# Kernel optimization log

Measured on AMD Instinct MI355X. Metric: run time of the kernel, lower is better.

The kernel has to match this reference:

```python
import jax, jax.numpy as jnp
import numpy as np

# ---- configuration (from init_kwargs / image geometry) ----
NUM_CLASSES = 10          # digit classes 1..10 (scores has K+1 cols, col 0 = background)
R = 500000                # total digit proposals for the image
T = 2048                  # topk_per_image: fixed-size survivor set for jit-friendly NMS
SCORE_T = 0.05            # digit_score_thresh
NMS_T = 0.5               # nms_thresh
IMG_W, IMG_H = 1920.0, 1080.0
CLS_OFFSET = IMG_W + IMG_H + 1.0  # batched_nms coordinate-offset trick (per-class NMS)


def setup_inputs() -> dict:
    key = jax.random.key(0)
    k1, k2, k3, k4 = jax.random.split(key, 4)
    # realistic boxes: uniform centers over the image, sizes in [10, 100] px
    cxcy = jax.random.uniform(k1, (R, 2)) * jnp.array([IMG_W, IMG_H], dtype=jnp.float32)
    wh = 10.0 + 90.0 * jax.random.uniform(k2, (R, 2))
    boxes = jnp.concatenate([cxcy - 0.5 * wh, cxcy + 0.5 * wh], axis=1)  # [R,4] x1y1x2y2
    # class probabilities over K+1 classes (col 0 = background)
    scores = jax.nn.softmax(jax.random.normal(k3, (R, NUM_CLASSES + 1)), axis=1)
    # per-box digit-center score (pred_digit_center_scores)
    center_scores = jax.random.uniform(k4, (R,))
    return {"boxes": boxes, "scores": scores, "center_scores": center_scores}


def _iou_matrix(b):
    # b: [T,4] in x1y1x2y2. Returns [T,T] pairwise IoU.
    area = jnp.clip(b[:, 2] - b[:, 0], 0.0) * jnp.clip(b[:, 3] - b[:, 1], 0.0)  # [T]
    lt = jnp.maximum(b[:, None, :2], b[None, :, :2])  # [T,T,2]
    rb = jnp.minimum(b[:, None, 2:], b[None, :, 2:])  # [T,T,2]
    wh = jnp.clip(rb - lt, 0.0)
    inter = wh[..., 0] * wh[..., 1]
    return inter / (area[:, None] + area[None, :] - inter + 1e-9)


def reference(boxes, scores, center_scores):
    # 1) drop background column, fuse with digit-center scores
    fg = scores[:, 1:] * center_scores[:, None]            # [R,K]
    # 2) clip boxes to image (Boxes.clip)
    clipped = jnp.stack([
        jnp.clip(boxes[:, 0], 0.0, IMG_W),
        jnp.clip(boxes[:, 1], 0.0, IMG_H),
        jnp.clip(boxes[:, 2], 0.0, IMG_W),
        jnp.clip(boxes[:, 3], 0.0, IMG_H),
    ], axis=1)                                             # [R,4]
    # 3) flatten (box, class) candidates and threshold (filter_mask = scores > thresh)
    flat = fg.reshape(-1)                                  # [R*K]
    masked = jnp.where(flat > SCORE_T, flat, -1.0)
    # 4) fixed-size pre-filter: top-T candidates by fused score
    vals, idx = jax.lax.top_k(masked, T)                   # sorted descending
    cand_boxes = clipped[idx // NUM_CLASSES]               # [T,4]
    cand_cls = idx % NUM_CLASSES                           # [T] (cls_id - 1)
    valid = vals > SCORE_T
    # 5) per-class batched NMS via coordinate-offset trick
    nms_boxes = cand_boxes + cand_cls.astype(cand_boxes.dtype)[:, None] * CLS_OFFSET
    iou = _iou_matrix(nms_boxes)                           # [T,T]
    rng = jnp.arange(T)
    def body(i, keep):
        sup = keep[i] & (iou[i] > NMS_T) & (rng > i)
        return keep & jnp.logical_not(sup)
    keep = jax.lax.fori_loop(0, T, body, valid)            # greedy NMS (inputs sorted by score)
    # 6) masked fixed-shape outputs: kept boxes + kept scores
    out_boxes = jnp.where(keep[:, None], cand_boxes, 0.0)
    out_scores = jnp.where(keep, vals, 0.0)
    return jnp.concatenate([out_boxes, out_scores[:, None]], axis=1)  # [T,5]
```

## Files before the change

### kernel.cpp

```cpp
#include <hip/hip_runtime.h>
#include <stdint.h>

typedef unsigned int u32;
typedef unsigned long long u64;

#define SCORE_THR 0.05f
#define NMS_THR   0.5f
#define TK        2048
#define CAP       4096
#define BASE14    ((int)(0x3D4CCCCDu >> 14))
#define MAGIC11   3123612579ull
#define NREP      8
#define PAIR_CAP  16384
#define SGRID     1024

#define WS_OFFS   0
#define WS_BINPOS 16384
#define WS_HDR    32768
#define WS_CBX    33024
#define WS_NBX    65792
#define WS_VALS   98560
#define WS_HREP   106752
#define WS_BUF    237824
#define WS_PAIRS  269824

__global__ void k_hist(const float* __restrict__ scores,
                       const float* __restrict__ center,
                       int R, u32* __restrict__ hrep) {
    __shared__ u32 h[4096];
    for (int t = threadIdx.x; t < 4096; t += blockDim.x) h[t] = 0;
    __syncthreads();
    int total_e = R * 11;
    int nq = total_e >> 2;
    int qpb = (nq + (int)gridDim.x - 1) / (int)gridDim.x;
    int start = (int)blockIdx.x * qpb;
    int end = start + qpb; if (end > nq) end = nq;
    int bd = (int)blockDim.x;
    for (int q = start + (int)threadIdx.x; q < end; q += 4 * bd) {
        int q1 = q + bd, q2 = q + 2 * bd, q3 = q + 3 * bd;
        float4 va, vb, vc, vd;
        bool ga = true, gb = q1 < end, gc = q2 < end, gd = q3 < end;
        va = ((const float4*)scores)[q];
        if (gb) vb = ((const float4*)scores)[q1];
        if (gc) vc = ((const float4*)scores)[q2];
        if (gd) vd = ((const float4*)scores)[q3];
#define HPROC(g, qq, v4)                                                   \
        if (g) {                                                           \
            float vv[4] = {v4.x, v4.y, v4.z, v4.w};                        \
            _Pragma("unroll")                                              \
            for (int j = 0; j < 4; j++) {                                  \
                u32 e2 = ((u32)(qq) << 2) + (u32)j;                        \
                u32 r = (u32)(((u64)e2 * MAGIC11) >> 35);                  \
                u32 c = e2 - r * 11u;                                      \
                if (c != 0u) {                                             \
                    float s = __fmul_rn(vv[j], center[r]);                 \
                    if (s > SCORE_THR) {                                   \
                        u32 key = __float_as_uint(s);                      \
                        int b = (int)(key >> 14) - BASE14;                 \
                        b = min(max(b, 0), 4095);                          \
                        atomicAdd(&h[b], 1u);                              \
                    }                                                      \
                }                                                          \
            }                                                              \
        }
        HPROC(ga, q, va) HPROC(gb, q1, vb) HPROC(gc, q2, vc) HPROC(gd, q3, vd)
#undef HPROC
    }
    if (blockIdx.x == 0 && threadIdx.x == 0) {
        for (int e2 = nq << 2; e2 < total_e; e2++) {
            u32 r = (u32)(((u64)(u32)e2 * MAGIC11) >> 35);
            u32 c = (u32)e2 - r * 11u;
            if (c != 0u) {
                float s = __fmul_rn(scores[e2], center[r]);
                if (s > SCORE_THR) {
                    u32 key = __float_as_uint(s);
                    int b = (int)(key >> 14) - BASE14;
                    b = min(max(b, 0), 4095);
                    atomicAdd(&h[b], 1u);
                }
            }
        }
    }
    __syncthreads();
    u32* hout = hrep + (size_t)(blockIdx.x & (NREP - 1)) * 4096;
    for (int t = threadIdx.x; t < 4096; t += blockDim.x)
        if (h[t]) atomicAdd(&hout[t], h[t]);
}

__global__ void k_scan(const u32* __restrict__ hrep, u32* __restrict__ offs,
                       u32* hdr) {
    int lane = threadIdx.x;
    int base = 4096 - 64 * (lane + 1);
    u32 v[64];
    u32 segsum = 0;
#pragma unroll
    for (int j = 0; j < 64; j++) {
        u32 s = 0;
#pragma unroll
        for (int i = 0; i < NREP; i++) s += hrep[i * 4096 + base + j];
        v[j] = s; segsum += s;
    }
    u32 incl = segsum;
    for (int off = 1; off < 64; off <<= 1) {
        u32 t = (u32)__shfl_up((int)incl, off);
        if (lane >= off) incl += t;
    }
    u32 excl = incl - segsum;
    u32 total = (u32)__shfl((int)incl, 63);
    u32 run = excl;
#pragma unroll
    for (int j = 63; j >= 0; j--) { offs[base + j] = run; run += v[j]; }
    if (lane == 0) hdr[6] = total;
    if (total < (u32)TK) {
        if (lane == 0) { hdr[3] = 0; hdr[5] = total; }
        return;
    }
    if ((excl < (u32)TK) && (incl >= (u32)TK)) {
        u32 cum = excl;
#pragma unroll
        for (int j = 63; j >= 0; j--) {
            u32 nc = cum + v[j];
            if (nc >= (u32)TK) { hdr[3] = (u32)(base + j); hdr[5] = nc; break; }
            cum = nc;
        }
    }
}

__global__ void k_collect(const float* __restrict__ scores,
                          const float* __restrict__ center,
                          int R, const u32* __restrict__ hdr,
                          const u32* __restrict__ offs, u32* __restrict__ binpos,
                          u64* __restrict__ buf) {
    u32 thr = hdr[3];
    int total_e = R * 11;
    int nq = total_e >> 2;
    int qpb = (nq + (int)gridDim.x - 1) / (int)gridDim.x;
    int start = (int)blockIdx.x * qpb;
    int end = start + qpb; if (end > nq) end = nq;
    int bd = (int)blockDim.x;
    for (int q = start + (int)threadIdx.x; q < end; q += 4 * bd) {
        int q1 = q + bd, q2 = q + 2 * bd, q3 = q + 3 * bd;
        float4 va, vb, vc, vd;
        bool ga = true, gb = q1 < end, gc = q2 < end, gd = q3 < end;
        va = ((const float4*)scores)[q];
        if (gb) vb = ((const float4*)scores)[q1];
        if (gc) vc = ((const float4*)scores)[q2];
        if (gd) vd = ((const float4*)scores)[q3];
#define CPROC(g, qq, v4)                                                   \
        if (g) {                                                           \
            float vv[4] = {v4.x, v4.y, v4.z, v4.w};                        \
            _Pragma("unroll")                                              \
            for (int j = 0; j < 4; j++) {                                  \
                u32 e2 = ((u32)(qq) << 2) + (u32)j;                        \
                u32 r = (u32)(((u64)e2 * MAGIC11) >> 35);                  \
                u32 c = e2 - r * 11u;                                      \
                if (c != 0u) {                                             \
                    float s = __fmul_rn(vv[j], center[r]);                 \
                    if (s > SCORE_THR) {                                   \
                        u32 key = __float_as_uint(s);                      \
                        int b = (int)(key >> 14) - BASE14;                 \
                        b = min(max(b, 0), 4095);                          \
                        if ((u32)b >= thr) {                               \
                            u32 slot = atomicAdd(&binpos[b], 1u);          \
                            u32 pos = offs[b] + slot;                      \
                            if (pos < CAP) {                               \
                                u32 idx = r * 10u + (c - 1u);              \
                                buf[pos] = ((u64)key << 32) | (u64)(~idx); \
                            }                                              \
                        }                                                  \
                    }                                                      \
                }                                                          \
            }                                                              \
        }
        CPROC(ga, q, va) CPROC(gb, q1, vb) CPROC(gc, q2, vc) CPROC(gd, q3, vd)
#undef CPROC
    }
    if (blockIdx.x == 0 && threadIdx.x == 0) {
        for (int e2 = nq << 2; e2 < total_e; e2++) {
            u32 r = (u32)(((u64)(u32)e2 * MAGIC11) >> 35);
            u32 c = (u32)e2 - r * 11u;
            if (c != 0u) {
                float s = __fmul_rn(scores[e2], center[r]);
                if (s > SCORE_THR) {
                    u32 key = __float_as_uint(s);
                    int b = (int)(key >> 14) - BASE14;
                    b = min(max(b, 0), 4095);
                    if ((u32)b >= thr) {
                        u32 slot = atomicAdd(&binpos[b], 1u);
                        u32 pos = offs[b] + slot;
                        if (pos < CAP) {
                            u32 idx = r * 10u + (c - 1u);
                            buf[pos] = ((u64)key << 32) | (u64)(~idx);
                        }
                    }
                }
            }
        }
    }
}

__global__ __launch_bounds__(1024) void k_rank(
        const float* __restrict__ boxes, const u32* __restrict__ offs,
        const u32* __restrict__ hdr, const u64* __restrict__ buf,
        float* __restrict__ cand_bx, float* __restrict__ nms_bx,
        float* __restrict__ vals) {
    __shared__ u64 kb[CAP];
    __shared__ u32 lo[4096];
    int tid = threadIdx.x;
    u32 n = hdr[5]; if (n > (u32)CAP) n = CAP;
    u32 total = hdr[6];
    for (int t = tid; t < CAP; t += 1024) kb[t] = (t < (int)n) ? buf[t] : 0ull;
    for (int t = tid; t < 4096; t += 1024) lo[t] = offs[t];
    __syncthreads();
    for (int i = tid; i < (int)n; i += 1024) {
        u64 x = kb[i];
        u32 key = (u32)(x >> 32);
        int b = (int)(key >> 14) - BASE14;
        b = min(max(b, 0), 4095);
        u32 start = lo[b];
        u32 end = (b > 0) ? lo[b - 1] : total;
        if (end > (u32)CAP) end = CAP;
        u32 rk = start;
        for (u32 j = start; j < end; j++) rk += (kb[j] > x) ? 1u : 0u;
        if (rk < (u32)TK) {
            u32 idx = ~(u32)x;
            u32 r = idx / 10u, cls = idx % 10u;
            const float* bp = boxes + (size_t)r * 4;
            float c0 = fminf(fmaxf(bp[0], 0.f), 1920.f);
            float c1 = fminf(fmaxf(bp[1], 0.f), 1080.f);
            float c2 = fminf(fmaxf(bp[2], 0.f), 1920.f);
            float c3 = fminf(fmaxf(bp[3], 0.f), 1080.f);
            float offv = __fmul_rn((float)cls, 3001.0f);
            cand_bx[rk * 4 + 0] = c0; cand_bx[rk * 4 + 1] = c1;
            cand_bx[rk * 4 + 2] = c2; cand_bx[rk * 4 + 3] = c3;
            nms_bx[rk * 4 + 0] = __fadd_rn(c0, offv);
            nms_bx[rk * 4 + 1] = __fadd_rn(c1, offv);
            nms_bx[rk * 4 + 2] = __fadd_rn(c2, offv);
            nms_bx[rk * 4 + 3] = __fadd_rn(c3, offv);
            vals[rk] = __uint_as_float(key);
        }
    }
}

__global__ void k_mask(const float* __restrict__ nms_bx, u32* __restrict__ hdr,
                       u32* __restrict__ pairs) {
    int colbase = blockIdx.x * 64, rowbase = blockIdx.y * 64;
    if (colbase + 63 <= rowbase) return;
    __shared__ float4 cb[64];
    __shared__ float ca[64];
    int tid = threadIdx.x;
    float4 c = ((const float4*)nms_bx)[colbase + tid];
    cb[tid] = c;
    ca[tid] = __fmul_rn(fmaxf(__fsub_rn(c.z, c.x), 0.f),
                        fmaxf(__fsub_rn(c.w, c.y), 0.f));
    int row = rowbase + tid;
    float4 rb = ((const float4*)nms_bx)[row];
    float rarea = __fmul_rn(fmaxf(__fsub_rn(rb.z, rb.x), 0.f),
                            fmaxf(__fsub_rn(rb.w, rb.y), 0.f));
    __syncthreads();
    for (int cc = 0; cc < 64; cc++) {
        int col = colbase + cc;
        if (col > row) {
            float4 cbv = cb[cc];
            float ltx = fmaxf(rb.x, cbv.x), lty = fmaxf(rb.y, cbv.y);
            float rbx = fminf(rb.z, cbv.z), rby = fminf(rb.w, cbv.w);
            float w = fmaxf(__fsub_rn(rbx, ltx), 0.f);
            float h = fmaxf(__fsub_rn(rby, lty), 0.f);
            float inter = __fmul_rn(w, h);
            float denom = __fadd_rn(__fsub_rn(__fadd_rn(rarea, ca[cc]), inter), 1e-9f);
            float iou = __fdiv_rn(inter, denom);
            if (iou > NMS_THR) {
                u32 p = atomicAdd(&hdr[8], 1u);
                if (p < PAIR_CAP)
                    pairs[p] = ((u32)row << 11) | (u32)col;
            }
        }
    }
}

__global__ __launch_bounds__(64) void k_final(
        const u32* __restrict__ pairs, const u32* __restrict__ hdr,
        const float* __restrict__ vals, const float* __restrict__ cand_bx,
        float* __restrict__ out) {
    __shared__ u32 sp[PAIR_CAP];
    __shared__ u32 cur[2048];
    int lane = threadIdx.x;
    u32 np = hdr[8]; if (np > (u32)PAIR_CAP) np = PAIR_CAP;
    const float4* vp = (const float4*)vals + (size_t)lane * 8;
    float4 vv[8];
#pragma unroll
    for (int j = 0; j < 8; j++) vv[j] = vp[j];
    u32 validw = 0;
#pragma unroll
    for (int j = 0; j < 8; j++) {
        validw |= (vv[j].x > SCORE_THR ? 1u : 0u) << (4 * j + 0);
        validw |= (vv[j].y > SCORE_THR ? 1u : 0u) << (4 * j + 1);
        validw |= (vv[j].z > SCORE_THR ? 1u : 0u) << (4 * j + 2);
        validw |= (vv[j].w > SCORE_THR ? 1u : 0u) << (4 * j + 3);
    }
    for (int t = lane; t < 2048; t += 64) cur[t] = 0;
    __syncthreads();
    for (u32 k = lane; k < np; k += 64) atomicAdd(&cur[pairs[k] >> 11], 1u);
    __syncthreads();
    u32 cnt[32];
    u32 seg = 0;
#pragma unroll
    for (int j = 0; j < 32; j++) { cnt[j] = cur[lane * 32 + j]; seg += cnt[j]; }
    u32 incl = seg;
    for (int off = 1; off < 64; off <<= 1) {
        u32 t = (u32)__shfl_up((int)incl, off);
        if (lane >= off) incl += t;
    }
    u32 run = incl - seg;
#pragma unroll
    for (int j = 0; j < 32; j++) { cur[lane * 32 + j] = run; run += cnt[j]; }
    __syncthreads();
    for (u32 k = lane; k < np; k += 64) {
        u32 p = pairs[k];
        u32 pos = atomicAdd(&cur[p >> 11], 1u);
        sp[pos] = p;
    }
    __syncthreads();
    u32 removed = 0;
    for (u32 k = 0; k < np; k++) {
        u32 p = sp[k];
        u32 row = p >> 11, col = p & 2047u;
        u32 aw = (u32)__shfl((int)(validw & ~removed), (int)(row >> 5));
        if ((aw >> (row & 31)) & 1u)
            if (lane == (int)(col >> 5)) removed |= 1u << (col & 31);
    }
    u32 keepw = validw & ~removed;
#pragma unroll
    for (int b = 0; b < 32; b++) {
        int i = lane * 32 + b;
        bool kp = (keepw >> b) & 1u;
        const float4 bx = ((const float4*)cand_bx)[i];
        float v = (b & 3) == 0 ? vv[b >> 2].x :
                  (b & 3) == 1 ? vv[b >> 2].y :
                  (b & 3) == 2 ? vv[b >> 2].z : vv[b >> 2].w;
        out[i * 5 + 0] = kp ? bx.x : 0.f;
        out[i * 5 + 1] = kp ? bx.y : 0.f;
        out[i * 5 + 2] = kp ? bx.z : 0.f;
        out[i * 5 + 3] = kp ? bx.w : 0.f;
        out[i * 5 + 4] = kp ? v : 0.f;
    }
}

extern "C" void kernel_launch(void* const* d_in, const int* in_sizes, int n_in,
                              void* d_out, int out_size, void* d_ws, size_t ws_size,
                              hipStream_t stream) {
    const float* boxes = (const float*)d_in[0];
    const float* scores = (const float*)d_in[1];
    const float* center = (const float*)d_in[2];
    float* out = (float*)d_out;
    int R = in_sizes[2];

    char* w = (char*)d_ws;
    u32* offs   = (u32*)(w + WS_OFFS);
    u32* binpos = (u32*)(w + WS_BINPOS);
    u32* hdr    = (u32*)(w + WS_HDR);
    float* cbx  = (float*)(w + WS_CBX);
    float* nbx  = (float*)(w + WS_NBX);
    float* vls  = (float*)(w + WS_VALS);
    u32* hrep   = (u32*)(w + WS_HREP);
    u64* buf    = (u64*)(w + WS_BUF);
    u32* pairs  = (u32*)(w + WS_PAIRS);

    hipMemsetAsync(w + WS_BINPOS, 0, WS_BUF - WS_BINPOS, stream);

    k_hist<<<SGRID, 256, 0, stream>>>(scores, center, R, hrep);
    k_scan<<<1, 64, 0, stream>>>(hrep, offs, hdr);
    k_collect<<<SGRID, 256, 0, stream>>>(scores, center, R, hdr, offs, binpos, buf);
    k_rank<<<1, 1024, 0, stream>>>(boxes, offs, hdr, buf, cbx, nbx, vls);
    k_mask<<<dim3(32, 32), 64, 0, stream>>>(nbx, hdr, pairs);
    k_final<<<1, 64, 0, stream>>>(pairs, hdr, vls, cbx, out);
}
```

Baseline: 141.6 us.

## Fuse six kernels into three using last-block-done tail work

Merges histogram+scan, collect+rank, and mask+final into three kernels, where the last block to finish (detected via an atomic counter in the header) performs the serial tail stage. This removes three kernel launches and their inter-kernel gaps. The tail stages now run with 256 or 64 threads instead of 1024 for rank, the sorted-pair buffer moves from shared memory to global workspace (reusing the histogram replica area), and the pair-processing loop batches 64 pairs per load with shuffles. It relies on correct release/acquire fencing across blocks and on the memset clearing the new counters.

```diff
diff --git a/kernel.cpp b/kernel.cpp
--- a/kernel.cpp
+++ b/kernel.cpp
@@ -24,10 +24,29 @@
 #define WS_BUF    237824
 #define WS_PAIRS  269824
 
-__global__ void k_hist(const float* __restrict__ scores,
-                       const float* __restrict__ center,
-                       int R, u32* __restrict__ hrep) {
+__device__ __forceinline__ u32 block_join(u32* cnt, u32 nb, u32* lastf_s) {
+    __syncthreads();
+    if (threadIdx.x == 0) {
+        u32 old = __hip_atomic_fetch_add(cnt, 1u, __ATOMIC_RELEASE,
+                                         __HIP_MEMORY_SCOPE_AGENT);
+        *lastf_s = (old == nb - 1u) ? 1u : 0u;
+    }
+    __syncthreads();
+    u32 l = *lastf_s;
+    if (l) {
+        if (threadIdx.x == 0) __threadfence();
+        __syncthreads();
+    }
+    return l;
+}
+
+__global__ void k_hist_scan(const float* __restrict__ scores,
+                            const float* __restrict__ center,
+                            int R, u32* __restrict__ hrep,
+                            u32* __restrict__ offs, u32* hdr) {
     __shared__ u32 h[4096];
+    __shared__ u32 wsum[4];
+    __shared__ u32 lastf;
     for (int t = threadIdx.x; t < 4096; t += blockDim.x) h[t] = 0;
     __syncthreads();
     int total_e = R * 11;
@@ -85,40 +104,45 @@
     u32* hout = hrep + (size_t)(blockIdx.x & (NREP - 1)) * 4096;
     for (int t = threadIdx.x; t < 4096; t += blockDim.x)
         if (h[t]) atomicAdd(&hout[t], h[t]);
-}
-
-__global__ void k_scan(const u32* __restrict__ hrep, u32* __restrict__ offs,
-                       u32* hdr) {
-    int lane = threadIdx.x;
-    int base = 4096 - 64 * (lane + 1);
-    u32 v[64];
+
+    if (!block_join(&hdr[16], gridDim.x, &lastf)) return;
+
+    int t = threadIdx.x;
+    int base = 4096 - 16 * (t + 1);
+    u32 v[16];
     u32 segsum = 0;
 #pragma unroll
-    for (int j = 0; j < 64; j++) {
+    for (int j = 0; j < 16; j++) {
         u32 s = 0;
 #pragma unroll
         for (int i = 0; i < NREP; i++) s += hrep[i * 4096 + base + j];
         v[j] = s; segsum += s;
     }
     u32 incl = segsum;
+#pragma unroll
     for (int off = 1; off < 64; off <<= 1) {
-        u32 t = (u32)__shfl_up((int)incl, off);
-        if (lane >= off) incl += t;
-    }
+        u32 x = (u32)__shfl_up((int)incl, off);
+        if ((t & 63) >= off) incl += x;
+    }
+    if ((t & 63) == 63) wsum[t >> 6] = incl;
+    __syncthreads();
+    u32 woff = 0;
+    for (int w = 0; w < (t >> 6); w++) woff += wsum[w];
+    u32 total = wsum[0] + wsum[1] + wsum[2] + wsum[3];
+    incl += woff;
     u32 excl = incl - segsum;
-    u32 total = (u32)__shfl((int)incl, 63);
     u32 run = excl;
 #pragma unroll
-    for (int j = 63; j >= 0; j--) { offs[base + j] = run; run += v[j]; }
-    if (lane == 0) hdr[6] = total;
+    for (int j = 15; j >= 0; j--) { offs[base + j] = run; run += v[j]; }
+    if (t == 0) hdr[6] = total;
     if (total < (u32)TK) {
-        if (lane == 0) { hdr[3] = 0; hdr[5] = total; }
+        if (t == 0) { hdr[3] = 0; hdr[5] = total; }
         return;
     }
     if ((excl < (u32)TK) && (incl >= (u32)TK)) {
         u32 cum = excl;
 #pragma unroll
-        for (int j = 63; j >= 0; j--) {
+        for (int j = 15; j >= 0; j--) {
             u32 nc = cum + v[j];
             if (nc >= (u32)TK) { hdr[3] = (u32)(base + j); hdr[5] = nc; break; }
             cum = nc;
@@ -126,11 +150,18 @@
     }
 }
 
-__global__ void k_collect(const float* __restrict__ scores,
-                          const float* __restrict__ center,
-                          int R, const u32* __restrict__ hdr,
-                          const u32* __restrict__ offs, u32* __restrict__ binpos,
-                          u64* __restrict__ buf) {
+__global__ void k_collect_rank(const float* __restrict__ scores,
+                               const float* __restrict__ center,
+                               const float* __restrict__ boxes,
+                               int R, u32* hdr,
+                               const u32* __restrict__ offs,
+                               u32* __restrict__ binpos,
+                               u64* __restrict__ buf,
+                               float* __restrict__ cand_bx,
+                               float* __restrict__ nms_bx,
+                               float* __restrict__ vals) {
+    __shared__ u64 kb[CAP];
+    __shared__ u32 lastf;
     u32 thr = hdr[3];
     int total_e = R * 11;
     int nq = total_e >> 2;
@@ -197,31 +228,24 @@
             }
         }
     }
-}
-
-__global__ __launch_bounds__(1024) void k_rank(
-        const float* __restrict__ boxes, const u32* __restrict__ offs,
-        const u32* __restrict__ hdr, const u64* __restrict__ buf,
-        float* __restrict__ cand_bx, float* __restrict__ nms_bx,
-        float* __restrict__ vals) {
-    __shared__ u64 kb[CAP];
-    __shared__ u32 lo[4096];
+
+    if (!block_join(&hdr[17], gridDim.x, &lastf)) return;
+
     int tid = threadIdx.x;
     u32 n = hdr[5]; if (n > (u32)CAP) n = CAP;
     u32 total = hdr[6];
-    for (int t = tid; t < CAP; t += 1024) kb[t] = (t < (int)n) ? buf[t] : 0ull;
-    for (int t = tid; t < 4096; t += 1024) lo[t] = offs[t];
-    __syncthreads();
-    for (int i = tid; i < (int)n; i += 1024) {
+    for (int t = tid; t < CAP; t += 256) kb[t] = (t < (int)n) ? buf[t] : 0ull;
+    __syncthreads();
+    for (int i = tid; i < (int)n; i += 256) {
         u64 x = kb[i];
         u32 key = (u32)(x >> 32);
         int b = (int)(key >> 14) - BASE14;
         b = min(max(b, 0), 4095);
-        u32 start = lo[b];
-        u32 end = (b > 0) ? lo[b - 1] : total;
-        if (end > (u32)CAP) end = CAP;
-        u32 rk = start;
-        for (u32 j = start; j < end; j++) rk += (kb[j] > x) ? 1u : 0u;
+        u32 bs = offs[b];
+        u32 be = (b > 0) ? offs[b - 1] : total;
+        if (be > (u32)CAP) be = CAP;
+        u32 rk = bs;
+        for (u32 j = bs; j < be; j++) rk += (kb[j] > x) ? 1u : 0u;
         if (rk < (u32)TK) {
             u32 idx = ~(u32)x;
             u32 r = idx / 10u, cls = idx % 10u;
@@ -242,49 +266,50 @@
     }
 }
 
-__global__ void k_mask(const float* __restrict__ nms_bx, u32* __restrict__ hdr,
-                       u32* __restrict__ pairs) {
-    int colbase = blockIdx.x * 64, rowbase = blockIdx.y * 64;
-    if (colbase + 63 <= rowbase) return;
+__global__ __launch_bounds__(64) void k_mask_final(
+        const float* __restrict__ nms_bx, u32* hdr, u32* __restrict__ pairs,
+        u32* __restrict__ spg,
+        const float* __restrict__ vals, const float* __restrict__ cand_bx,
+        float* __restrict__ out) {
     __shared__ float4 cb[64];
     __shared__ float ca[64];
-    int tid = threadIdx.x;
-    float4 c = ((const float4*)nms_bx)[colbase + tid];
-    cb[tid] = c;
-    ca[tid] = __fmul_rn(fmaxf(__fsub_rn(c.z, c.x), 0.f),
-                        fmaxf(__fsub_rn(c.w, c.y), 0.f));
-    int row = rowbase + tid;
-    float4 rb = ((const float4*)nms_bx)[row];
-    float rarea = __fmul_rn(fmaxf(__fsub_rn(rb.z, rb.x), 0.f),
-                            fmaxf(__fsub_rn(rb.w, rb.y), 0.f));
-    __syncthreads();
-    for (int cc = 0; cc < 64; cc++) {
-        int col = colbase + cc;
-        if (col > row) {
-            float4 cbv = cb[cc];
-            float ltx = fmaxf(rb.x, cbv.x), lty = fmaxf(rb.y, cbv.y);
-            float rbx = fminf(rb.z, cbv.z), rby = fminf(rb.w, cbv.w);
-            float w = fmaxf(__fsub_rn(rbx, ltx), 0.f);
-            float h = fmaxf(__fsub_rn(rby, lty), 0.f);
-            float inter = __fmul_rn(w, h);
-            float denom = __fadd_rn(__fsub_rn(__fadd_rn(rarea, ca[cc]), inter), 1e-9f);
-            float iou = __fdiv_rn(inter, denom);
-            if (iou > NMS_THR) {
-                u32 p = atomicAdd(&hdr[8], 1u);
-                if (p < PAIR_CAP)
-                    pairs[p] = ((u32)row << 11) | (u32)col;
+    __shared__ u32 cur[2048];
+    __shared__ u32 lastf;
+    int colbase = blockIdx.x * 64, rowbase = blockIdx.y * 64;
+    int lane = threadIdx.x;
+    if (colbase + 63 > rowbase) {
+        float4 c = ((const float4*)nms_bx)[colbase + lane];
+        cb[lane] = c;
+        ca[lane] = __fmul_rn(fmaxf(__fsub_rn(c.z, c.x), 0.f),
+                             fmaxf(__fsub_rn(c.w, c.y), 0.f));
+        int row = rowbase + lane;
+        float4 rb = ((const float4*)nms_bx)[row];
+        float rarea = __fmul_rn(fmaxf(__fsub_rn(rb.z, rb.x), 0.f),
+                                fmaxf(__fsub_rn(rb.w, rb.y), 0.f));
+        __syncthreads();
+        for (int cc = 0; cc < 64; cc++) {
+            int col = colbase + cc;
+            if (col > row) {
+                float4 cbv = cb[cc];
+                float ltx = fmaxf(rb.x, cbv.x), lty = fmaxf(rb.y, cbv.y);
+                float rbx = fminf(rb.z, cbv.z), rby = fminf(rb.w, cbv.w);
+                float w = fmaxf(__fsub_rn(rbx, ltx), 0.f);
+                float h = fmaxf(__fsub_rn(rby, lty), 0.f);
+                float inter = __fmul_rn(w, h);
+                float denom = __fadd_rn(__fsub_rn(__fadd_rn(rarea, ca[cc]),
+                                                  inter), 1e-9f);
+                float iou = __fdiv_rn(inter, denom);
+                if (iou > NMS_THR) {
+                    u32 p = atomicAdd(&hdr[8], 1u);
+                    if (p < PAIR_CAP)
+                        pairs[p] = ((u32)row << 11) | (u32)col;
+                }
             }
         }
     }
-}
-
-__global__ __launch_bounds__(64) void k_final(
-        const u32* __restrict__ pairs, const u32* __restrict__ hdr,
-        const float* __restrict__ vals, const float* __restrict__ cand_bx,
-        float* __restrict__ out) {
-    __shared__ u32 sp[PAIR_CAP];
-    __shared__ u32 cur[2048];
-    int lane = threadIdx.x;
+
+    if (!block_join(&hdr[18], gridDim.x * gridDim.y, &lastf)) return;
+
     u32 np = hdr[8]; if (np > (u32)PAIR_CAP) np = PAIR_CAP;
     const float4* vp = (const float4*)vals + (size_t)lane * 8;
     float4 vv[8];
@@ -318,16 +343,20 @@
     for (u32 k = lane; k < np; k += 64) {
         u32 p = pairs[k];
         u32 pos = atomicAdd(&cur[p >> 11], 1u);
-        sp[pos] = p;
+        spg[pos] = p;
     }
     __syncthreads();
     u32 removed = 0;
-    for (u32 k = 0; k < np; k++) {
-        u32 p = sp[k];
-        u32 row = p >> 11, col = p & 2047u;
-        u32 aw = (u32)__shfl((int)(validw & ~removed), (int)(row >> 5));
-        if ((aw >> (row & 31)) & 1u)
-            if (lane == (int)(col >> 5)) removed |= 1u << (col & 31);
+    for (u32 k0 = 0; k0 < np; k0 += 64) {
+        u32 myp = (k0 + (u32)lane < np) ? spg[k0 + lane] : 0u;
+        u32 c2 = np - k0; if (c2 > 64u) c2 = 64u;
+        for (u32 s2 = 0; s2 < c2; s2++) {
+            u32 p = (u32)__shfl((int)myp, (int)s2);
+            u32 row = p >> 11, col = p & 2047u;
+            u32 aw = (u32)__shfl((int)(validw & ~removed), (int)(row >> 5));
+            if ((aw >> (row & 31)) & 1u)
+                if (lane == (int)(col >> 5)) removed |= 1u << (col & 31);
+        }
     }
     u32 keepw = validw & ~removed;
 #pragma unroll
@@ -368,10 +397,10 @@
 
     hipMemsetAsync(w + WS_BINPOS, 0, WS_BUF - WS_BINPOS, stream);
 
-    k_hist<<<SGRID, 256, 0, stream>>>(scores, center, R, hrep);
-    k_scan<<<1, 64, 0, stream>>>(hrep, offs, hdr);
-    k_collect<<<SGRID, 256, 0, stream>>>(scores, center, R, hdr, offs, binpos, buf);
-    k_rank<<<1, 1024, 0, stream>>>(boxes, offs, hdr, buf, cbx, nbx, vls);
-    k_mask<<<dim3(32, 32), 64, 0, stream>>>(nbx, hdr, pairs);
-    k_final<<<1, 64, 0, stream>>>(pairs, hdr, vls, cbx, out);
+    k_hist_scan<<<SGRID, 256, 0, stream>>>(scores, center, R, hrep, offs, hdr);
+    k_collect_rank<<<SGRID, 256, 0, stream>>>(scores, center, boxes, R, hdr,
+                                              offs, binpos, buf, cbx, nbx, vls);
+    k_mask_final<<<dim3(32, 32), 64, 0, stream>>>(nbx, hdr, pairs,
+                                                  (u32*)(w + WS_HREP),
+                                                  vls, cbx, out);
 }
```

Measured after the change: 164.8 us. 16.4% more time.
